# Performance work log

Hardware: AMD Instinct MI355X
Metric: run time of the kernel (lower is better)

## Reference

```python
import jax, jax.numpy as jnp
import numpy as np

DIM = 192
HEADS = 16
DIM_HEAD = 64
INNER = HEADS * DIM_HEAD  # 1024
B, N = 8, 1024


def setup_inputs() -> dict:
    key = jax.random.key(0)
    ks = jax.random.split(key, 8)
    x = jax.random.normal(ks[0], (B, N, DIM), dtype=jnp.float32)
    shift = jax.random.normal(ks[1], (B, 1, DIM), dtype=jnp.float32)
    scale = jax.random.normal(ks[2], (B, 1, DIM), dtype=jnp.float32)
    norm_w = jnp.ones((DIM,), dtype=jnp.float32)
    norm_b = jnp.zeros((DIM,), dtype=jnp.float32)
    w_qkv = jax.random.normal(ks[3], (DIM, 3 * INNER), dtype=jnp.float32) * (DIM ** -0.5)
    w_out = jax.random.normal(ks[4], (INNER, DIM), dtype=jnp.float32) * (INNER ** -0.5)
    b_out = jnp.zeros((DIM,), dtype=jnp.float32)
    return {"x": x, "shift": shift, "scale": scale, "norm_w": norm_w,
            "norm_b": norm_b, "w_qkv": w_qkv, "w_out": w_out, "b_out": b_out}


def _layernorm(x, w, b, eps=1e-5):
    mu = jnp.mean(x, axis=-1, keepdims=True)
    var = jnp.mean(jnp.square(x - mu), axis=-1, keepdims=True)
    return (x - mu) * jax.lax.rsqrt(var + eps) * w + b


def reference(x, shift, scale, norm_w, norm_b, w_qkv, w_out, b_out):
    h = _layernorm(x, norm_w, norm_b)
    h = h * (1.0 + scale) + shift  # adaLN modulation, broadcast over tokens
    qkv = h @ w_qkv  # [B, N, 3*INNER]
    q, k, v = jnp.split(qkv, 3, axis=-1)
    # [B, N, INNER] -> [B, H, N, Dh]
    def split_heads(t):
        return t.reshape(B, N, HEADS, DIM_HEAD).transpose(0, 2, 1, 3)
    q, k, v = split_heads(q), split_heads(k), split_heads(v)
    scores = jnp.einsum('bhnd,bhmd->bhnm', q, k) * (DIM_HEAD ** -0.5)
    attn = jax.nn.softmax(scores, axis=-1)
    out = jnp.einsum('bhnm,bhmd->bhnd', attn, v)  # [B, H, N, Dh]
    out = out.transpose(0, 2, 1, 3).reshape(B, N, INNER)
    return out @ w_out + b_out
```

## Files before the change

### kernel.cpp

```cpp
#include <hip/hip_runtime.h>

#define DIM 192
#define NB 8
#define NTOK 1024
#define HEADS 16
#define DH 64
#define INNER 1024
#define ROWS (NB * NTOK)

typedef __bf16 bf16x8 __attribute__((ext_vector_type(8)));
typedef float f32x4 __attribute__((ext_vector_type(4)));
typedef float f32x16 __attribute__((ext_vector_type(16)));
typedef unsigned int u32x4 __attribute__((ext_vector_type(4)));

__device__ inline unsigned short f2bf(float f) {
    union { float f; unsigned u; } v; v.f = f;
    unsigned r = v.u + 0x7FFF + ((v.u >> 16) & 1);
    return (unsigned short)(r >> 16);
}

__device__ inline unsigned pk2(float a, float b) {
    __bf16 x = (__bf16)a, y = (__bf16)b;
    unsigned short ux = __builtin_bit_cast(unsigned short, x);
    unsigned short uy = __builtin_bit_cast(unsigned short, y);
    return (unsigned)ux | ((unsigned)uy << 16);
}

__device__ inline void gl_lds16(const unsigned short* g, unsigned short* l) {
    __builtin_amdgcn_global_load_lds(
        (const __attribute__((address_space(1))) void*)g,
        (__attribute__((address_space(3))) void*)l, 16, 0, 0);
}

__device__ inline size_t fragIdx(int row, int k, int depth) {
    return ((size_t)(row >> 5) * ((size_t)depth * 4) +
            (size_t)(((k >> 4) * 2 + ((k >> 3) & 1)) * 32 + (row & 31))) * 8 + (k & 7);
}

__global__ __launch_bounds__(256) void k_pre(
    const float* __restrict__ x, const float* __restrict__ shift,
    const float* __restrict__ scale, const float* __restrict__ nw,
    const float* __restrict__ nb, const float* __restrict__ wqkv,
    const float* __restrict__ wout,
    unsigned short* __restrict__ hF, unsigned short* __restrict__ wF,
    unsigned short* __restrict__ woF) {
    int bid = blockIdx.x;
    if (bid < 2048) {
        int row = bid * 4 + (threadIdx.x >> 6);
        int lane = threadIdx.x & 63;
        const float* xr = x + row * DIM;
        float v0 = xr[lane], v1 = xr[lane + 64], v2 = xr[lane + 128];
        float s = v0 + v1 + v2;
        #pragma unroll
        for (int m = 1; m < 64; m <<= 1) s += __shfl_xor(s, m);
        float mean = s * (1.0f / DIM);
        float d0 = v0 - mean, d1 = v1 - mean, d2 = v2 - mean;
        float q = d0 * d0 + d1 * d1 + d2 * d2;
        #pragma unroll
        for (int m = 1; m < 64; m <<= 1) q += __shfl_xor(q, m);
        float rs = rsqrtf(q * (1.0f / DIM) + 1e-5f);
        int b = row >> 10;
        float vv[3] = {v0, v1, v2};
        #pragma unroll
        for (int i = 0; i < 3; i++) {
            int d = lane + 64 * i;
            float val = (vv[i] - mean) * rs * nw[d] + nb[d];
            val = val * (1.0f + scale[b * DIM + d]) + shift[b * DIM + d];
            hF[fragIdx(row, d, DIM)] = f2bf(val);
        }
    } else if (bid < 4352) {
        int idx = (bid - 2048) * 256 + threadIdx.x;
        int k = idx / 3072, c = idx % 3072;
        wF[fragIdx(c, k, DIM)] = f2bf(wqkv[idx]);
    } else {
        int idx = (bid - 4352) * 256 + threadIdx.x;
        int k = idx / 192, c = idx % 192;
        woF[fragIdx(c, k, INNER)] = f2bf(wout[idx]);
    }
}

__global__ __launch_bounds__(256, 3) void k_qkv(
    const unsigned short* __restrict__ hF, const unsigned short* __restrict__ wF,
    unsigned short* __restrict__ qm, unsigned short* __restrict__ km,
    unsigned short* __restrict__ vtm) {
    const float QSC = 0.125f * 1.4426950408889634f;
    int tid = threadIdx.x;
    int wave = tid >> 6, lane = tid & 63;
    int l31 = lane & 31, hi = lane >> 5;
    int c0 = blockIdx.x * 64 + (wave >> 1) * 32;
    int typ = c0 >> 10;
    int hd  = (c0 & 1023) >> 6;
    int coff = c0 & 32;

    const unsigned short* Ab = wF + (size_t)(c0 >> 5) * 768 * 8;
    bf16x8 af[12];
    #pragma unroll
    for (int kc = 0; kc < 12; kc++)
        af[kc] = *(const bf16x8*)(Ab + ((kc * 2 + hi) * 32 + l31) * 8);

    #pragma unroll
    for (int ns = 0; ns < 2; ns++) {
        int n0 = blockIdx.y * 128 + (wave & 1) * 64 + ns * 32;
        const unsigned short* Bb = hF + (size_t)(n0 >> 5) * 768 * 8;
        f32x16 acc0, acc1;
        #pragma unroll
        for (int r = 0; r < 16; r++) { acc0[r] = 0.f; acc1[r] = 0.f; }
        #pragma unroll
        for (int kc = 0; kc < 6; kc++) {
            bf16x8 bf0 = *(const bf16x8*)(Bb + (((2 * kc) * 2 + hi) * 32 + l31) * 8);
            bf16x8 bf1 = *(const bf16x8*)(Bb + (((2 * kc + 1) * 2 + hi) * 32 + l31) * 8);
            acc0 = __builtin_amdgcn_mfma_f32_32x32x16_bf16(af[2 * kc], bf0, acc0, 0, 0, 0);
            acc1 = __builtin_amdgcn_mfma_f32_32x32x16_bf16(af[2 * kc + 1], bf1, acc1, 0, 0, 0);
        }
        f32x16 acc;
        #pragma unroll
        for (int r = 0; r < 16; r++) acc[r] = acc0[r] + acc1[r];
        int n = n0 + l31, bb = n >> 10, nm = n & 1023;
        if (typ < 2) {
            float sc = (typ == 0) ? QSC : 1.0f;
            unsigned short* base = (typ == 0 ? qm : km) +
                ((size_t)(bb * 16 + hd) * 1024 + nm) * 64;
            #pragma unroll
            for (int rg = 0; rg < 4; rg++) {
                uint2 val;
                val.x = pk2(acc[rg * 4 + 0] * sc, acc[rg * 4 + 1] * sc);
                val.y = pk2(acc[rg * 4 + 2] * sc, acc[rg * 4 + 3] * sc);
                *(uint2*)(base + coff + rg * 8 + hi * 4) = val;
            }
        } else {
            unsigned short* base = vtm + (size_t)(bb * 16 + hd) * 65536 + nm;
            #pragma unroll
            for (int r = 0; r < 16; r++) {
                int d = coff + (r & 3) + 8 * (r >> 2) + 4 * hi;
                base[(size_t)d * 1024] = f2bf(acc[r]);
            }
        }
    }
}

__global__ __launch_bounds__(256, 4) void k_attn(
    const unsigned short* __restrict__ qm, const unsigned short* __restrict__ km,
    const unsigned short* __restrict__ vtm, unsigned short* __restrict__ attnF) {
    __shared__ __align__(128) unsigned short Kb[2][4096];
    __shared__ __align__(128) unsigned short Vb[3][4096];

    int tid = threadIdx.x;
    int wave = tid >> 6, lane = tid & 63;
    int l31 = lane & 31, hi = lane >> 5;
    int bh = blockIdx.x, qt = blockIdx.y;
    int qbase = qt * 128 + wave * 32;
    const unsigned short* Q = qm + (size_t)bh * NTOK * DH;
    const unsigned short* K = km + (size_t)bh * NTOK * DH;
    const unsigned short* VT = vtm + (size_t)bh * DH * NTOK;

    bf16x8 qf[4];
    #pragma unroll
    for (int c = 0; c < 4; c++)
        qf[c] = *(const bf16x8*)(Q + (qbase + l31) * DH + c * 16 + hi * 8);

    u32x4 ov; ov[0] = 0x3F803F80u; ov[1] = 0x3F803F80u; ov[2] = 0x3F803F80u; ov[3] = 0x3F803F80u;
    bf16x8 ones = __builtin_bit_cast(bf16x8, ov);

    f32x16 accO[2], accL;
    #pragma unroll
    for (int r = 0; r < 16; r++) { accO[0][r] = 0.f; accO[1][r] = 0.f; accL[r] = 0.f; }

    auto stageK = [&](int b, int t) {
        #pragma unroll
        for (int r = 0; r < 2; r++) {
            int off = (tid + r * 256) * 16;
            int row = off >> 7, col = off & 127;
            int scol = col ^ ((row & 7) << 4);
            gl_lds16(K + (t * 64 + row) * DH + (scol >> 1),
                     (unsigned short*)((char*)Kb[b] + off));
        }
    };
    auto stageV = [&](int b, int t) {
        #pragma unroll
        for (int r = 0; r < 2; r++) {
            int off = (tid + r * 256) * 16;
            int row = off >> 7, col = off & 127;
            int scol = col ^ ((row & 7) << 4);
            gl_lds16(VT + (size_t)row * NTOK + t * 64 + (scol >> 1),
                     (unsigned short*)((char*)Vb[b] + off));
        }
    };
    auto ldK = [&](int b, int row, int col) -> bf16x8 {
        int scol = col ^ ((row & 7) << 4);
        return *(const bf16x8*)((const char*)Kb[b] + row * 128 + scol);
    };
    auto ldV = [&](int b, int row, int col) -> bf16x8 {
        int scol = col ^ ((row & 7) << 4);
        return *(const bf16x8*)((const char*)Vb[b] + row * 128 + scol);
    };
    auto packP = [&](const f32x16& P, bf16x8& w0, bf16x8& w1) {
        u32x4 A, B;
        {
            auto r0 = __builtin_amdgcn_permlane32_swap(pk2(P[0], P[1]), pk2(P[4], P[5]), false, false);
            auto r1 = __builtin_amdgcn_permlane32_swap(pk2(P[2], P[3]), pk2(P[6], P[7]), false, false);
            A[0] = r0[0]; A[1] = r1[0]; A[2] = r0[1]; A[3] = r1[1];
        }
        {
            auto r0 = __builtin_amdgcn_permlane32_swap(pk2(P[8], P[9]), pk2(P[12], P[13]), false, false);
            auto r1 = __builtin_amdgcn_permlane32_swap(pk2(P[10], P[11]), pk2(P[14], P[15]), false, false);
            B[0] = r0[0]; B[1] = r1[0]; B[2] = r0[1]; B[3] = r1[1];
        }
        w0 = __builtin_bit_cast(bf16x8, A);
        w1 = __builtin_bit_cast(bf16x8, B);
    };

    bf16x8 pw[4];

    stageK(0, 0); stageV(0, 0);
    __syncthreads();

    stageK(1, 1); stageV(1, 1);
    {
        f32x16 C0, C1;
        #pragma unroll
        for (int r = 0; r < 16; r++) { C0[r] = 0.f; C1[r] = 0.f; }
        __builtin_amdgcn_s_setprio(1);
        #pragma unroll
        for (int c = 0; c < 4; c++) {
            bf16x8 kf = ldK(0, l31, c * 32 + hi * 16);
            C0 = __builtin_amdgcn_mfma_f32_32x32x16_bf16(kf, qf[c], C0, 0, 0, 0);
            bf16x8 kf2 = ldK(0, 32 + l31, c * 32 + hi * 16);
            C1 = __builtin_amdgcn_mfma_f32_32x32x16_bf16(kf2, qf[c], C1, 0, 0, 0);
        }
        __builtin_amdgcn_s_setprio(0);
        #pragma unroll
        for (int r = 0; r < 16; r++) {
            C0[r] = __builtin_amdgcn_exp2f(C0[r]);
            C1[r] = __builtin_amdgcn_exp2f(C1[r]);
        }
        packP(C0, pw[0], pw[1]);
        packP(C1, pw[2], pw[3]);
        #pragma unroll
        for (int kcc = 0; kcc < 4; kcc++)
            accL = __builtin_amdgcn_mfma_f32_32x32x16_bf16(ones, pw[kcc], accL, 0, 0, 0);
        __syncthreads();
    }

    for (int t = 1; t < 16; t++) {
        int kc = t & 1;
        int vp = (t - 1) % 3;
        if (t < 15) { stageK((t + 1) & 1, t + 1); stageV((t + 1) % 3, t + 1); }

        f32x16 C0, C1;
        #pragma unroll
        for (int r = 0; r < 16; r++) { C0[r] = 0.f; C1[r] = 0.f; }
        __builtin_amdgcn_s_setprio(1);
        #pragma unroll
        for (int c = 0; c < 4; c++) {
            bf16x8 kf = ldK(kc, l31, c * 32 + hi * 16);
            C0 = __builtin_amdgcn_mfma_f32_32x32x16_bf16(kf, qf[c], C0, 0, 0, 0);
            bf16x8 kf2 = ldK(kc, 32 + l31, c * 32 + hi * 16);
            C1 = __builtin_amdgcn_mfma_f32_32x32x16_bf16(kf2, qf[c], C1, 0, 0, 0);
        }
        #pragma unroll
        for (int dt = 0; dt < 2; dt++) {
            #pragma unroll
            for (int kcc = 0; kcc < 4; kcc++) {
                bf16x8 vf = ldV(vp, dt * 32 + l31, kcc * 32 + hi * 16);
                accO[dt] = __builtin_amdgcn_mfma_f32_32x32x16_bf16(vf, pw[kcc], accO[dt], 0, 0, 0);
            }
        }
        __builtin_amdgcn_s_setprio(0);

        #pragma unroll
        for (int r = 0; r < 16; r++) {
            C0[r] = __builtin_amdgcn_exp2f(C0[r]);
            C1[r] = __builtin_amdgcn_exp2f(C1[r]);
        }
        packP(C0, pw[0], pw[1]);
        packP(C1, pw[2], pw[3]);
        #pragma unroll
        for (int kcc = 0; kcc < 4; kcc++)
            accL = __builtin_amdgcn_mfma_f32_32x32x16_bf16(ones, pw[kcc], accL, 0, 0, 0);
        __syncthreads();
    }

    __builtin_amdgcn_s_setprio(1);
    #pragma unroll
    for (int dt = 0; dt < 2; dt++) {
        #pragma unroll
        for (int kcc = 0; kcc < 4; kcc++) {
            bf16x8 vf = ldV(0, dt * 32 + l31, kcc * 32 + hi * 16);
            accO[dt] = __builtin_amdgcn_mfma_f32_32x32x16_bf16(vf, pw[kcc], accO[dt], 0, 0, 0);
        }
    }
    __builtin_amdgcn_s_setprio(0);

    float inv = 1.0f / accL[0];
    int b = bh >> 4, hd = bh & 15;
    int rowblk = b * 32 + qt * 4 + wave;
    #pragma unroll
    for (int dt = 0; dt < 2; dt++)
        #pragma unroll
        for (int rq = 0; rq < 4; rq++) {
            int g = (hd * 4 + dt * 2 + (rq >> 1)) * 2 + (rq & 1);
            uint2 val;
            val.x = pk2(accO[dt][rq * 4 + 0] * inv, accO[dt][rq * 4 + 1] * inv);
            val.y = pk2(accO[dt][rq * 4 + 2] * inv, accO[dt][rq * 4 + 3] * inv);
            *(uint2*)((char*)attnF + ((size_t)rowblk * 4096 + g * 32 + l31) * 16 + hi * 8) = val;
        }
}

__global__ __launch_bounds__(256, 2) void k_out(
    const unsigned short* __restrict__ attnF, const unsigned short* __restrict__ woF,
    const float* __restrict__ bias, float* __restrict__ out) {
    int wave = threadIdx.x >> 6, lane = threadIdx.x & 63;
    int l31 = lane & 31, hi = lane >> 5;
    int W = blockIdx.x * 4 + wave;
    int nb = W / 6, cb = W % 6;
    const unsigned short* A = attnF + (size_t)nb * 4096 * 8;
    const unsigned short* B = woF + (size_t)cb * 4096 * 8;

    f32x16 acc0, acc1;
    #pragma unroll
    for (int r = 0; r < 16; r++) { acc0[r] = 0.f; acc1[r] = 0.f; }
    #pragma unroll 8
    for (int kc = 0; kc < 32; kc++) {
        bf16x8 a0 = *(const bf16x8*)(A + (((2 * kc) * 2 + hi) * 32 + l31) * 8);
        bf16x8 b0 = *(const bf16x8*)(B + (((2 * kc) * 2 + hi) * 32 + l31) * 8);
        bf16x8 a1 = *(const bf16x8*)(A + (((2 * kc + 1) * 2 + hi) * 32 + l31) * 8);
        bf16x8 b1 = *(const bf16x8*)(B + (((2 * kc + 1) * 2 + hi) * 32 + l31) * 8);
        acc0 = __builtin_amdgcn_mfma_f32_32x32x16_bf16(a0, b0, acc0, 0, 0, 0);
        acc1 = __builtin_amdgcn_mfma_f32_32x32x16_bf16(a1, b1, acc1, 0, 0, 0);
    }
    float bi = bias[cb * 32 + l31];
    #pragma unroll
    for (int r = 0; r < 16; r++) {
        int n = nb * 32 + (r & 3) + 8 * (r >> 2) + 4 * hi;
        out[(size_t)n * DIM + cb * 32 + l31] = acc0[r] + acc1[r] + bi;
    }
}

extern "C" void kernel_launch(void* const* d_in, const int* in_sizes, int n_in,
                              void* d_out, int out_size, void* d_ws, size_t ws_size,
                              hipStream_t stream) {
    const float* x     = (const float*)d_in[0];
    const float* shift = (const float*)d_in[1];
    const float* scale = (const float*)d_in[2];
    const float* nw    = (const float*)d_in[3];
    const float* nbv   = (const float*)d_in[4];
    const float* wqkv  = (const float*)d_in[5];
    const float* wout  = (const float*)d_in[6];
    const float* bout  = (const float*)d_in[7];
    float* out = (float*)d_out;

    char* ws = (char*)d_ws;
    unsigned short* hF    = (unsigned short*)(ws + 0);
    unsigned short* wF    = (unsigned short*)(ws + 3145728);
    unsigned short* woF   = (unsigned short*)(ws + 3145728 + 1179648);
    unsigned short* qm    = (unsigned short*)(ws + 4718592);
    unsigned short* km    = (unsigned short*)(ws + 4718592 + 16777216);
    unsigned short* vtm   = (unsigned short*)(ws + 4718592 + 2 * 16777216);
    unsigned short* attnF = (unsigned short*)(ws + 4718592 + 3 * 16777216);

    k_pre<<<dim3(5120), dim3(256), 0, stream>>>(x, shift, scale, nw, nbv, wqkv, wout, hF, wF, woF);
    k_qkv<<<dim3(48, 64), dim3(256), 0, stream>>>(hF, wF, qm, km, vtm);
    k_attn<<<dim3(128, 8), dim3(256), 0, stream>>>(qm, km, vtm, attnF);
    k_out<<<dim3(384), dim3(256), 0, stream>>>(attnF, woF, bout, out);
}
```

Measured before the change: 98.90 us.

## Store Q/K/V in MFMA fragment layout and read directly from global in attention

New measurement: 90.84 us, median of 2. 1.09x faster.

```diff
diff --git a/kernel.cpp b/kernel.cpp
--- a/kernel.cpp
+++ b/kernel.cpp
@@ -24,12 +24,6 @@
     unsigned short ux = __builtin_bit_cast(unsigned short, x);
     unsigned short uy = __builtin_bit_cast(unsigned short, y);
     return (unsigned)ux | ((unsigned)uy << 16);
-}
-
-__device__ inline void gl_lds16(const unsigned short* g, unsigned short* l) {
-    __builtin_amdgcn_global_load_lds(
-        (const __attribute__((address_space(1))) void*)g,
-        (__attribute__((address_space(3))) void*)l, 16, 0, 0);
 }
 
 __device__ inline size_t fragIdx(int row, int k, int depth) {
@@ -81,8 +75,8 @@
 
 __global__ __launch_bounds__(256, 3) void k_qkv(
     const unsigned short* __restrict__ hF, const unsigned short* __restrict__ wF,
-    unsigned short* __restrict__ qm, unsigned short* __restrict__ km,
-    unsigned short* __restrict__ vtm) {
+    unsigned short* __restrict__ qmF, unsigned short* __restrict__ kmF,
+    unsigned short* __restrict__ vtF) {
     const float QSC = 0.125f * 1.4426950408889634f;
     int tid = threadIdx.x;
     int wave = tid >> 6, lane = tid & 63;
@@ -105,93 +99,89 @@
         f32x16 acc0, acc1;
         #pragma unroll
         for (int r = 0; r < 16; r++) { acc0[r] = 0.f; acc1[r] = 0.f; }
-        #pragma unroll
-        for (int kc = 0; kc < 6; kc++) {
-            bf16x8 bf0 = *(const bf16x8*)(Bb + (((2 * kc) * 2 + hi) * 32 + l31) * 8);
-            bf16x8 bf1 = *(const bf16x8*)(Bb + (((2 * kc + 1) * 2 + hi) * 32 + l31) * 8);
-            acc0 = __builtin_amdgcn_mfma_f32_32x32x16_bf16(af[2 * kc], bf0, acc0, 0, 0, 0);
-            acc1 = __builtin_amdgcn_mfma_f32_32x32x16_bf16(af[2 * kc + 1], bf1, acc1, 0, 0, 0);
+        if (typ < 2) {
+            #pragma unroll
+            for (int kc = 0; kc < 6; kc++) {
+                bf16x8 bf0 = *(const bf16x8*)(Bb + (((2 * kc) * 2 + hi) * 32 + l31) * 8);
+                bf16x8 bf1 = *(const bf16x8*)(Bb + (((2 * kc + 1) * 2 + hi) * 32 + l31) * 8);
+                acc0 = __builtin_amdgcn_mfma_f32_32x32x16_bf16(af[2 * kc], bf0, acc0, 0, 0, 0);
+                acc1 = __builtin_amdgcn_mfma_f32_32x32x16_bf16(af[2 * kc + 1], bf1, acc1, 0, 0, 0);
+            }
+        } else {
+            #pragma unroll
+            for (int kc = 0; kc < 6; kc++) {
+                bf16x8 bf0 = *(const bf16x8*)(Bb + (((2 * kc) * 2 + hi) * 32 + l31) * 8);
+                bf16x8 bf1 = *(const bf16x8*)(Bb + (((2 * kc + 1) * 2 + hi) * 32 + l31) * 8);
+                acc0 = __builtin_amdgcn_mfma_f32_32x32x16_bf16(bf0, af[2 * kc], acc0, 0, 0, 0);
+                acc1 = __builtin_amdgcn_mfma_f32_32x32x16_bf16(bf1, af[2 * kc + 1], acc1, 0, 0, 0);
+            }
         }
         f32x16 acc;
         #pragma unroll
         for (int r = 0; r < 16; r++) acc[r] = acc0[r] + acc1[r];
-        int n = n0 + l31, bb = n >> 10, nm = n & 1023;
+
+        int bb = n0 >> 10, nm = n0 & 1023;
+        int tt = nm >> 6;
+        unsigned short* base;
+        if (typ == 0) base = qmF + (size_t)(bb * 16 + hd) * 65536;
+        else if (typ == 1) base = kmF + (size_t)(bb * 16 + hd) * 65536;
+        else base = vtF + (size_t)(bb * 16 + hd) * 65536;
+
         if (typ < 2) {
             float sc = (typ == 0) ? QSC : 1.0f;
-            unsigned short* base = (typ == 0 ? qm : km) +
-                ((size_t)(bb * 16 + hd) * 1024 + nm) * 64;
+            int rowgrp = (nm >> 5) & 1;
             #pragma unroll
             for (int rg = 0; rg < 4; rg++) {
+                int ob = coff + rg * 8;
+                int g = (rowgrp * 4 + (ob >> 4)) * 2 + ((ob >> 3) & 1);
                 uint2 val;
                 val.x = pk2(acc[rg * 4 + 0] * sc, acc[rg * 4 + 1] * sc);
                 val.y = pk2(acc[rg * 4 + 2] * sc, acc[rg * 4 + 3] * sc);
-                *(uint2*)(base + coff + rg * 8 + hi * 4) = val;
+                *(uint2*)(base + (tt * 16 + g) * 256 + l31 * 8 + hi * 4) = val;
             }
         } else {
-            unsigned short* base = vtm + (size_t)(bb * 16 + hd) * 65536 + nm;
-            #pragma unroll
-            for (int r = 0; r < 16; r++) {
-                int d = coff + (r & 3) + 8 * (r >> 2) + 4 * hi;
-                base[(size_t)d * 1024] = f2bf(acc[r]);
-            }
-        }
-    }
-}
-
-__global__ __launch_bounds__(256, 4) void k_attn(
-    const unsigned short* __restrict__ qm, const unsigned short* __restrict__ km,
-    const unsigned short* __restrict__ vtm, unsigned short* __restrict__ attnF) {
-    __shared__ __align__(128) unsigned short Kb[2][4096];
-    __shared__ __align__(128) unsigned short Vb[3][4096];
-
+            int drg = coff >> 5;
+            #pragma unroll
+            for (int rg = 0; rg < 4; rg++) {
+                int nb2 = (nm & 32) + rg * 8;
+                int g = (drg * 4 + (nb2 >> 4)) * 2 + ((nb2 >> 3) & 1);
+                uint2 val;
+                val.x = pk2(acc[rg * 4 + 0], acc[rg * 4 + 1]);
+                val.y = pk2(acc[rg * 4 + 2], acc[rg * 4 + 3]);
+                *(uint2*)(base + (tt * 16 + g) * 256 + l31 * 8 + hi * 4) = val;
+            }
+        }
+    }
+}
+
+__global__ __launch_bounds__(256, 3) void k_attn(
+    const unsigned short* __restrict__ qmF, const unsigned short* __restrict__ kmF,
+    const unsigned short* __restrict__ vtF, unsigned short* __restrict__ attnF) {
     int tid = threadIdx.x;
     int wave = tid >> 6, lane = tid & 63;
     int l31 = lane & 31, hi = lane >> 5;
     int bh = blockIdx.x, qt = blockIdx.y;
     int qbase = qt * 128 + wave * 32;
-    const unsigned short* Q = qm + (size_t)bh * NTOK * DH;
-    const unsigned short* K = km + (size_t)bh * NTOK * DH;
-    const unsigned short* VT = vtm + (size_t)bh * DH * NTOK;
-
+    const unsigned short* Qb = qmF + (size_t)bh * 65536;
+    const unsigned short* Kb = kmF + (size_t)bh * 65536;
+    const unsigned short* Vb = vtF + (size_t)bh * 65536;
+
+    int tq = qbase >> 6, rq = (qbase >> 5) & 1;
     bf16x8 qf[4];
     #pragma unroll
     for (int c = 0; c < 4; c++)
-        qf[c] = *(const bf16x8*)(Q + (qbase + l31) * DH + c * 16 + hi * 8);
-
-    u32x4 ov; ov[0] = 0x3F803F80u; ov[1] = 0x3F803F80u; ov[2] = 0x3F803F80u; ov[3] = 0x3F803F80u;
-    bf16x8 ones = __builtin_bit_cast(bf16x8, ov);
-
-    f32x16 accO[2], accL;
-    #pragma unroll
-    for (int r = 0; r < 16; r++) { accO[0][r] = 0.f; accO[1][r] = 0.f; accL[r] = 0.f; }
-
-    auto stageK = [&](int b, int t) {
-        #pragma unroll
-        for (int r = 0; r < 2; r++) {
-            int off = (tid + r * 256) * 16;
-            int row = off >> 7, col = off & 127;
-            int scol = col ^ ((row & 7) << 4);
-            gl_lds16(K + (t * 64 + row) * DH + (scol >> 1),
-                     (unsigned short*)((char*)Kb[b] + off));
-        }
+        qf[c] = *(const bf16x8*)(Qb + (tq * 16 + (rq * 4 + c) * 2 + hi) * 256 + l31 * 8);
+
+    float lsum = 0.f;
+    f32x16 accO[2];
+    #pragma unroll
+    for (int r = 0; r < 16; r++) { accO[0][r] = 0.f; accO[1][r] = 0.f; }
+
+    auto ldKf = [&](int t, int rowgrp, int c) -> bf16x8 {
+        return *(const bf16x8*)(Kb + (t * 16 + (rowgrp * 4 + c) * 2 + hi) * 256 + l31 * 8);
     };
-    auto stageV = [&](int b, int t) {
-        #pragma unroll
-        for (int r = 0; r < 2; r++) {
-            int off = (tid + r * 256) * 16;
-            int row = off >> 7, col = off & 127;
-            int scol = col ^ ((row & 7) << 4);
-            gl_lds16(VT + (size_t)row * NTOK + t * 64 + (scol >> 1),
-                     (unsigned short*)((char*)Vb[b] + off));
-        }
-    };
-    auto ldK = [&](int b, int row, int col) -> bf16x8 {
-        int scol = col ^ ((row & 7) << 4);
-        return *(const bf16x8*)((const char*)Kb[b] + row * 128 + scol);
-    };
-    auto ldV = [&](int b, int row, int col) -> bf16x8 {
-        int scol = col ^ ((row & 7) << 4);
-        return *(const bf16x8*)((const char*)Vb[b] + row * 128 + scol);
+    auto ldVf = [&](int t, int dt, int nc) -> bf16x8 {
+        return *(const bf16x8*)(Vb + (t * 16 + (dt * 4 + nc) * 2 + hi) * 256 + l31 * 8);
     };
     auto packP = [&](const f32x16& P, bf16x8& w0, bf16x8& w1) {
         u32x4 A, B;
@@ -208,13 +198,16 @@
         w0 = __builtin_bit_cast(bf16x8, A);
         w1 = __builtin_bit_cast(bf16x8, B);
     };
+    auto tsum = [](const f32x16& P) -> float {
+        float s0 = (P[0] + P[1]) + (P[2] + P[3]);
+        float s1 = (P[4] + P[5]) + (P[6] + P[7]);
+        float s2 = (P[8] + P[9]) + (P[10] + P[11]);
+        float s3 = (P[12] + P[13]) + (P[14] + P[15]);
+        return (s0 + s1) + (s2 + s3);
+    };
 
     bf16x8 pw[4];
 
-    stageK(0, 0); stageV(0, 0);
-    __syncthreads();
-
-    stageK(1, 1); stageV(1, 1);
     {
         f32x16 C0, C1;
         #pragma unroll
@@ -222,10 +215,8 @@
         __builtin_amdgcn_s_setprio(1);
         #pragma unroll
         for (int c = 0; c < 4; c++) {
-            bf16x8 kf = ldK(0, l31, c * 32 + hi * 16);
-            C0 = __builtin_amdgcn_mfma_f32_32x32x16_bf16(kf, qf[c], C0, 0, 0, 0);
-            bf16x8 kf2 = ldK(0, 32 + l31, c * 32 + hi * 16);
-            C1 = __builtin_amdgcn_mfma_f32_32x32x16_bf16(kf2, qf[c], C1, 0, 0, 0);
+            C0 = __builtin_amdgcn_mfma_f32_32x32x16_bf16(ldKf(0, 0, c), qf[c], C0, 0, 0, 0);
+            C1 = __builtin_amdgcn_mfma_f32_32x32x16_bf16(ldKf(0, 1, c), qf[c], C1, 0, 0, 0);
         }
         __builtin_amdgcn_s_setprio(0);
         #pragma unroll
@@ -233,36 +224,27 @@
             C0[r] = __builtin_amdgcn_exp2f(C0[r]);
             C1[r] = __builtin_amdgcn_exp2f(C1[r]);
         }
+        lsum += tsum(C0) + tsum(C1);
         packP(C0, pw[0], pw[1]);
         packP(C1, pw[2], pw[3]);
-        #pragma unroll
-        for (int kcc = 0; kcc < 4; kcc++)
-            accL = __builtin_amdgcn_mfma_f32_32x32x16_bf16(ones, pw[kcc], accL, 0, 0, 0);
-        __syncthreads();
     }
 
     for (int t = 1; t < 16; t++) {
-        int kc = t & 1;
-        int vp = (t - 1) % 3;
-        if (t < 15) { stageK((t + 1) & 1, t + 1); stageV((t + 1) % 3, t + 1); }
-
         f32x16 C0, C1;
         #pragma unroll
         for (int r = 0; r < 16; r++) { C0[r] = 0.f; C1[r] = 0.f; }
         __builtin_amdgcn_s_setprio(1);
         #pragma unroll
         for (int c = 0; c < 4; c++) {
-            bf16x8 kf = ldK(kc, l31, c * 32 + hi * 16);
-            C0 = __builtin_amdgcn_mfma_f32_32x32x16_bf16(kf, qf[c], C0, 0, 0, 0);
-            bf16x8 kf2 = ldK(kc, 32 + l31, c * 32 + hi * 16);
-            C1 = __builtin_amdgcn_mfma_f32_32x32x16_bf16(kf2, qf[c], C1, 0, 0, 0);
+            C0 = __builtin_amdgcn_mfma_f32_32x32x16_bf16(ldKf(t, 0, c), qf[c], C0, 0, 0, 0);
+            C1 = __builtin_amdgcn_mfma_f32_32x32x16_bf16(ldKf(t, 1, c), qf[c], C1, 0, 0, 0);
         }
         #pragma unroll
         for (int dt = 0; dt < 2; dt++) {
             #pragma unroll
-            for (int kcc = 0; kcc < 4; kcc++) {
-                bf16x8 vf = ldV(vp, dt * 32 + l31, kcc * 32 + hi * 16);
-                accO[dt] = __builtin_amdgcn_mfma_f32_32x32x16_bf16(vf, pw[kcc], accO[dt], 0, 0, 0);
+            for (int nc = 0; nc < 4; nc++) {
+                accO[dt] = __builtin_amdgcn_mfma_f32_32x32x16_bf16(
+                    ldVf(t - 1, dt, nc), pw[nc], accO[dt], 0, 0, 0);
             }
         }
         __builtin_amdgcn_s_setprio(0);
@@ -272,36 +254,33 @@
             C0[r] = __builtin_amdgcn_exp2f(C0[r]);
             C1[r] = __builtin_amdgcn_exp2f(C1[r]);
         }
+        lsum += tsum(C0) + tsum(C1);
         packP(C0, pw[0], pw[1]);
         packP(C1, pw[2], pw[3]);
-        #pragma unroll
-        for (int kcc = 0; kcc < 4; kcc++)
-            accL = __builtin_amdgcn_mfma_f32_32x32x16_bf16(ones, pw[kcc], accL, 0, 0, 0);
-        __syncthreads();
     }
 
     __builtin_amdgcn_s_setprio(1);
     #pragma unroll
     for (int dt = 0; dt < 2; dt++) {
         #pragma unroll
-        for (int kcc = 0; kcc < 4; kcc++) {
-            bf16x8 vf = ldV(0, dt * 32 + l31, kcc * 32 + hi * 16);
-            accO[dt] = __builtin_amdgcn_mfma_f32_32x32x16_bf16(vf, pw[kcc], accO[dt], 0, 0, 0);
+        for (int nc = 0; nc < 4; nc++) {
+            accO[dt] = __builtin_amdgcn_mfma_f32_32x32x16_bf16(
+                ldVf(15, dt, nc), pw[nc], accO[dt], 0, 0, 0);
         }
     }
     __builtin_amdgcn_s_setprio(0);
 
-    float inv = 1.0f / accL[0];
+    float inv = 1.0f / (lsum + __shfl_xor(lsum, 32));
     int b = bh >> 4, hd = bh & 15;
     int rowblk = b * 32 + qt * 4 + wave;
     #pragma unroll
     for (int dt = 0; dt < 2; dt++)
         #pragma unroll
-        for (int rq = 0; rq < 4; rq++) {
-            int g = (hd * 4 + dt * 2 + (rq >> 1)) * 2 + (rq & 1);
+        for (int rg = 0; rg < 4; rg++) {
+            int g = (hd * 4 + dt * 2 + (rg >> 1)) * 2 + (rg & 1);
             uint2 val;
-            val.x = pk2(accO[dt][rq * 4 + 0] * inv, accO[dt][rq * 4 + 1] * inv);
-            val.y = pk2(accO[dt][rq * 4 + 2] * inv, accO[dt][rq * 4 + 3] * inv);
+            val.x = pk2(accO[dt][rg * 4 + 0] * inv, accO[dt][rg * 4 + 1] * inv);
+            val.y = pk2(accO[dt][rg * 4 + 2] * inv, accO[dt][rg * 4 + 3] * inv);
             *(uint2*)((char*)attnF + ((size_t)rowblk * 4096 + g * 32 + l31) * 16 + hi * 8) = val;
         }
 }
@@ -353,13 +332,13 @@
     unsigned short* hF    = (unsigned short*)(ws + 0);
     unsigned short* wF    = (unsigned short*)(ws + 3145728);
     unsigned short* woF   = (unsigned short*)(ws + 3145728 + 1179648);
-    unsigned short* qm    = (unsigned short*)(ws + 4718592);
-    unsigned short* km    = (unsigned short*)(ws + 4718592 + 16777216);
-    unsigned short* vtm   = (unsigned short*)(ws + 4718592 + 2 * 16777216);
+    unsigned short* qmF   = (unsigned short*)(ws + 4718592);
+    unsigned short* kmF   = (unsigned short*)(ws + 4718592 + 16777216);
+    unsigned short* vtF   = (unsigned short*)(ws + 4718592 + 2 * 16777216);
     unsigned short* attnF = (unsigned short*)(ws + 4718592 + 3 * 16777216);
 
     k_pre<<<dim3(5120), dim3(256), 0, stream>>>(x, shift, scale, nw, nbv, wqkv, wout, hF, wF, woF);
-    k_qkv<<<dim3(48, 64), dim3(256), 0, stream>>>(hF, wF, qm, km, vtm);
-    k_attn<<<dim3(128, 8), dim3(256), 0, stream>>>(qm, km, vtm, attnF);
+    k_qkv<<<dim3(48, 64), dim3(256), 0, stream>>>(hF, wF, qmF, kmF, vtF);
+    k_attn<<<dim3(128, 8), dim3(256), 0, stream>>>(qmF, kmF, vtF, attnF);
     k_out<<<dim3(384), dim3(256), 0, stream>>>(attnF, woF, bout, out);
 }
```
